# Performance work log

Measured on AMD Instinct MI355X. Metric: run time of the kernel, lower is better.

Reference implementation:

```python
import jax, jax.numpy as jnp
import numpy as np

B, N, EB, NA, DIM, NIT = 256, 128, 5, 64, 512, 3  # EB = n_bonds + 1 (channel 0 = no-bond, dropped)


def setup_inputs() -> dict:
    key = jax.random.key(0)
    ks = jax.random.split(key, 10)
    adj = jax.random.uniform(ks[0], (B, N, N, EB), dtype=jnp.float32)
    node = jax.random.normal(ks[1], (B, N, NA), dtype=jnp.float32)
    hidden = jnp.zeros((B, N, DIM), dtype=jnp.float32)  # accepted but unused by forward
    # nn.Linear default init: U(-1/sqrt(fan_in), 1/sqrt(fan_in))
    se = 1.0 / np.sqrt(NA)
    sd = 1.0 / np.sqrt(DIM)
    W_embed = jax.random.uniform(ks[2], (NA, DIM), minval=-se, maxval=se, dtype=jnp.float32)
    b_embed = jax.random.uniform(ks[3], (DIM,), minval=-se, maxval=se, dtype=jnp.float32)
    W_layers = jax.random.uniform(ks[4], (NIT, DIM, DIM), minval=-sd, maxval=sd, dtype=jnp.float32)
    b_layers = jax.random.uniform(ks[5], (NIT, DIM), minval=-sd, maxval=sd, dtype=jnp.float32)
    W_out = jax.random.uniform(ks[6], (DIM, 1), minval=-sd, maxval=sd, dtype=jnp.float32)
    b_out = jax.random.uniform(ks[7], (1,), minval=-sd, maxval=sd, dtype=jnp.float32)
    return {"adj": adj, "hidden": hidden, "node": node,
            "W_embed": W_embed, "b_embed": b_embed,
            "W_layers": W_layers, "b_layers": b_layers,
            "W_out": W_out, "b_out": b_out}


def reference(adj, hidden, node, W_embed, b_embed, W_layers, b_layers, W_out, b_out):
    # adj[:, :, :, 1:].permute(0, 3, 1, 2) -> [B, E, N, N]
    a = jnp.transpose(adj[..., 1:], (0, 3, 1, 2))
    h = node @ W_embed + b_embed  # [B, N, DIM]
    for i in range(NIT):  # WLSLinearLayer: relu(Linear(h + sum_e adj_e @ h))
        agg = jnp.einsum('benm,bmd->bnd', a, h)  # sum over bond types of neighbor aggregation
        h = jax.nn.relu((h + agg) @ W_layers[i] + b_layers[i])
    graph_repr = jnp.mean(h, axis=1)  # [B, DIM]
    logit = graph_repr @ W_out + b_out  # [B, 1], activation=None path
    return (logit, graph_repr)
```

## Files before the change

### kernel.cpp

```cpp
#include <hip/hip_runtime.h>
#include <hip/hip_bf16.h>


typedef __bf16 bf16;
typedef __bf16 bf16x4 __attribute__((ext_vector_type(4)));
typedef __bf16 bf16x8 __attribute__((ext_vector_type(8)));
typedef float floatx4 __attribute__((ext_vector_type(4)));


__global__ __launch_bounds__(256) void k_pack(const float* __restrict__ We,
                                              const float* __restrict__ Wl,
                                              bf16* __restrict__ PWe,
                                              bf16* __restrict__ PWl) {
    __shared__ float S[512][17];
    int z = blockIdx.y, td = blockIdx.x;
    const float* src; bf16* dst; int K;
    if (z < 3) { src = Wl + (size_t)z * 262144; dst = PWl + (size_t)z * 262144; K = 512; }
    else       { src = We;                      dst = PWe;                      K = 64; }
    int tid = threadIdx.x;
    int x = tid & 15, y = tid >> 4;
    for (int kb = 0; kb < K; kb += 16) {
        int k = kb + y;
        S[k][x] = src[(size_t)k * 512 + td * 16 + x];
    }
    __syncthreads();
    int lane = tid & 63, w = tid >> 6, q = lane >> 4, l16 = lane & 15;
    int KT = K >> 5;
    for (int tk = w; tk < KT; tk += 4) {
        bf16x8 v;
#pragma unroll
        for (int j = 0; j < 8; j++) v[j] = (bf16)S[tk * 32 + q * 8 + j][l16];
        *(bf16x8*)&dst[(size_t)((td * KT + tk) * 64 + lane) * 8] = v;
    }
}

__global__ __launch_bounds__(1024, 4) void k_mega(
    const float* __restrict__ adj,
    const float* __restrict__ nodef,
    const bf16* __restrict__ PWe,
    const float* __restrict__ b_embed,
    const bf16* __restrict__ PWl,
    const float* __restrict__ b_layers,
    const float* __restrict__ W_out,
    const float* __restrict__ b_out,
    float* __restrict__ out)
{
    __shared__ __align__(16) char pool[163840];
    bf16* HT = (bf16*)pool;
    bf16* AhatP = (bf16*)(pool + 131072);

    const int b = blockIdx.x;
    const int tid = threadIdx.x;
    const int lane = tid & 63, wid = tid >> 6;
    const int q = lane >> 4, l16 = lane & 15;

    {
        const float4* srcb = (const float4*)(adj + (size_t)b * 81920);
#pragma unroll
        for (int p = 0; p < 4; p++) {
            int t = p * 1024 + tid;
            const float4* ptr = srcb + (size_t)t * 5;
            float4 v0 = ptr[0], v1 = ptr[1], v2 = ptr[2], v3 = ptr[3], v4 = ptr[4];
            float s0 = v0.y + v0.z + v0.w + v1.x;
            float s1 = v1.z + v1.w + v2.x + v2.y;
            float s2 = v2.w + v3.x + v3.y + v3.z;
            float s3 = v4.x + v4.y + v4.z + v4.w;
            int n = t >> 5, m0 = (t & 31) * 4;
            bf16x4 o;
            o[0] = (bf16)(s0 + ((n == m0 + 0) ? 1.f : 0.f));
            o[1] = (bf16)(s1 + ((n == m0 + 1) ? 1.f : 0.f));
            o[2] = (bf16)(s2 + ((n == m0 + 2) ? 1.f : 0.f));
            o[3] = (bf16)(s3 + ((n == m0 + 3) ? 1.f : 0.f));
            int ntG = n >> 4, l16n = n & 15;
            int kk = m0 >> 5, mq = (m0 & 31) >> 3, half = (m0 >> 2) & 1;
            int cphys = mq * 16 + (l16n ^ (mq * 2));
            *(bf16x4*)&AhatP[(size_t)(((ntG * 4 + kk) * 64 + cphys) * 8 + half * 4)] = o;
        }
    }

    {
        const float* Ab = nodef + (size_t)b * 8192;
        floatx4 accE[8][2] = {};
#pragma unroll
        for (int kk = 0; kk < 2; kk++) {
            bf16x8 bfr[2];
#pragma unroll
            for (int nt = 0; nt < 2; nt++)
                bfr[nt] = *(const bf16x8*)&PWe[(size_t)(((wid * 2 + nt) * 2 + kk) * 64 + lane) * 8];
#pragma unroll
            for (int half = 0; half < 2; half++) {
                bf16x8 af[4];
#pragma unroll
                for (int mt = 0; mt < 4; mt++) {
                    const float* srcp = Ab + (size_t)((half * 4 + mt) * 16 + l16) * 64 + kk * 32 + q * 8;
                    float4 x = *(const float4*)srcp;
                    float4 y = *(const float4*)(srcp + 4);
                    bf16x8 v;
                    v[0] = (bf16)x.x; v[1] = (bf16)x.y; v[2] = (bf16)x.z; v[3] = (bf16)x.w;
                    v[4] = (bf16)y.x; v[5] = (bf16)y.y; v[6] = (bf16)y.z; v[7] = (bf16)y.w;
                    af[mt] = v;
                }
#pragma unroll
                for (int mt = 0; mt < 4; mt++)
#pragma unroll
                    for (int nt = 0; nt < 2; nt++)
                        accE[half * 4 + mt][nt] = __builtin_amdgcn_mfma_f32_16x16x32_bf16(af[mt], bfr[nt], accE[half * 4 + mt][nt], 0, 0, 0);
            }
        }
#pragma unroll
        for (int nt = 0; nt < 2; nt++) {
            int d = wid * 32 + nt * 16 + l16;
            float bv = b_embed[d];
#pragma unroll
            for (int mt = 0; mt < 8; mt++) {
                int c = mt * 2 + (q >> 1);
                int off = ((c ^ (d & 15)) << 3) + (q & 1) * 4;
                bf16x4 pk;
#pragma unroll
                for (int r = 0; r < 4; r++) pk[r] = (bf16)(accE[mt][nt][r] + bv);
                *(bf16x4*)&HT[d * 128 + off] = pk;
            }
        }
    }
    __syncthreads();

    const int pc = lane ^ ((lane >> 4) * 2);

    for (int it = 0; it < 3; it++) {
        const bf16* WT = PWl + (size_t)it * 262144;
        const float* bl = b_layers + it * 512;

        const bf16* Wb0 = WT + (size_t)(wid * 2 + 0) * 8192 + lane * 8;
        const bf16* Wb1 = WT + (size_t)(wid * 2 + 1) * 8192 + lane * 8;

        bf16x8 w00 = *(const bf16x8*)Wb0;
        bf16x8 w01 = *(const bf16x8*)Wb1;
        bf16x8 w10 = *(const bf16x8*)(Wb0 + 512);
        bf16x8 w11 = *(const bf16x8*)(Wb1 + 512);

        floatx4 at[2][8] = {};
#pragma unroll
        for (int kk = 0; kk < 4; kk++) {
            bf16x8 afr[2];
#pragma unroll
            for (int dt = 0; dt < 2; dt++) {
                int drow = wid * 32 + dt * 16 + l16;
                int off = ((4 * kk + q) ^ (drow & 15)) << 3;
                afr[dt] = *(const bf16x8*)&HT[drow * 128 + off];
            }
#pragma unroll
            for (int g = 0; g < 2; g++) {
                bf16x8 bfr[4];
#pragma unroll
                for (int nt = 0; nt < 4; nt++)
                    bfr[nt] = *(const bf16x8*)&AhatP[(size_t)(((g * 4 + nt) * 4 + kk) * 64 + pc) * 8];
                __builtin_amdgcn_s_setprio(1);
#pragma unroll
                for (int nt = 0; nt < 4; nt++)
#pragma unroll
                    for (int dt = 0; dt < 2; dt++)
                        at[dt][g * 4 + nt] = __builtin_amdgcn_mfma_f32_16x16x32_bf16(afr[dt], bfr[nt], at[dt][g * 4 + nt], 0, 0, 0);
                __builtin_amdgcn_s_setprio(0);
            }
        }
        {
            bf16* Treg = HT + wid * 4096;
#pragma unroll
            for (int dt = 0; dt < 2; dt++)
#pragma unroll
                for (int nt = 0; nt < 8; nt++) {
                    int n = nt * 16 + l16;
                    bf16x4 pk;
#pragma unroll
                    for (int r = 0; r < 4; r++) pk[r] = (bf16)at[dt][nt][r];
                    *(bf16x4*)&Treg[(dt * 2 + (q >> 1)) * 1024 + n * 8 + (q & 1) * 4] = pk;
                }
        }
        __syncthreads();

        floatx4 acc[8][2] = {};
        for (int dc = 0; dc < 16; dc++) {
            int dcn = (dc + 2) & 15;
            bf16x8 n0 = *(const bf16x8*)(Wb0 + dcn * 512);
            bf16x8 n1 = *(const bf16x8*)(Wb1 + dcn * 512);
            const bf16* Tdc = HT + dc * 4096 + q * 1024 + l16 * 8;
            bf16x8 afa[4];
#pragma unroll
            for (int mt = 0; mt < 4; mt++)
                afa[mt] = *(const bf16x8*)&Tdc[mt * 128];
            __builtin_amdgcn_s_setprio(1);
#pragma unroll
            for (int mt = 0; mt < 4; mt++)
                acc[mt][0] = __builtin_amdgcn_mfma_f32_16x16x32_bf16(afa[mt], w00, acc[mt][0], 0, 0, 0);
#pragma unroll
            for (int mt = 0; mt < 4; mt++)
                acc[mt][1] = __builtin_amdgcn_mfma_f32_16x16x32_bf16(afa[mt], w01, acc[mt][1], 0, 0, 0);
            __builtin_amdgcn_s_setprio(0);
            bf16x8 afb[4];
#pragma unroll
            for (int mt = 0; mt < 4; mt++)
                afb[mt] = *(const bf16x8*)&Tdc[(mt + 4) * 128];
            __builtin_amdgcn_s_setprio(1);
#pragma unroll
            for (int mt = 0; mt < 4; mt++)
                acc[mt + 4][0] = __builtin_amdgcn_mfma_f32_16x16x32_bf16(afb[mt], w00, acc[mt + 4][0], 0, 0, 0);
#pragma unroll
            for (int mt = 0; mt < 4; mt++)
                acc[mt + 4][1] = __builtin_amdgcn_mfma_f32_16x16x32_bf16(afb[mt], w01, acc[mt + 4][1], 0, 0, 0);
            __builtin_amdgcn_s_setprio(0);
            w00 = w10; w01 = w11; w10 = n0; w11 = n1;
        }

        if (it < 2) {
            __syncthreads();
#pragma unroll
            for (int nt = 0; nt < 2; nt++) {
                int dp = wid * 32 + nt * 16 + l16;
                float bv = bl[dp];
#pragma unroll
                for (int mt = 0; mt < 8; mt++) {
                    int c = mt * 2 + (q >> 1);
                    int off = ((c ^ (dp & 15)) << 3) + (q & 1) * 4;
                    bf16x4 pk;
#pragma unroll
                    for (int r = 0; r < 4; r++) pk[r] = (bf16)fmaxf(acc[mt][nt][r] + bv, 0.f);
                    *(bf16x4*)&HT[dp * 128 + off] = pk;
                }
            }
        } else {
            float* RsF = (float*)(pool + 131072);
#pragma unroll
            for (int nt = 0; nt < 2; nt++) {
                int dp = wid * 32 + nt * 16 + l16;
                float bv = bl[dp];
                float s = 0.f;
#pragma unroll
                for (int mt = 0; mt < 8; mt++)
#pragma unroll
                    for (int r = 0; r < 4; r++)
                        s += fmaxf(acc[mt][nt][r] + bv, 0.f);
                s += __shfl_down(s, 32);
                s += __shfl_down(s, 16);
                if (lane < 16) RsF[dp] = s;
            }
        }
    }
    __syncthreads();

    float* RsF = (float*)(pool + 131072);
    float* lpF = (float*)(pool + 131072 + 2048);
    if (tid < 512) {
        float g = RsF[tid] * (1.f / 128.f);
        out[256 + (size_t)b * 512 + tid] = g;
        lpF[tid] = g * W_out[tid];
    }
    __syncthreads();
    if (wid == 0) {
        float s = 0.f;
#pragma unroll
        for (int k = 0; k < 8; k++) s += lpF[lane + k * 64];
        s += __shfl_down(s, 32);
        s += __shfl_down(s, 16);
        s += __shfl_down(s, 8);
        s += __shfl_down(s, 4);
        s += __shfl_down(s, 2);
        s += __shfl_down(s, 1);
        if (lane == 0) out[b] = s + b_out[0];
    }
}

extern "C" void kernel_launch(void* const* d_in, const int* in_sizes, int n_in,
                              void* d_out, int out_size, void* d_ws, size_t ws_size,
                              hipStream_t stream) {
    const float* adj      = (const float*)d_in[0];
    const float* node     = (const float*)d_in[2];
    const float* W_embed  = (const float*)d_in[3];
    const float* b_embed  = (const float*)d_in[4];
    const float* W_layers = (const float*)d_in[5];
    const float* b_layers = (const float*)d_in[6];
    const float* W_out    = (const float*)d_in[7];
    const float* b_out    = (const float*)d_in[8];
    float* out = (float*)d_out;

    char* ws = (char*)d_ws;
    bf16* PWe = (bf16*)(ws);
    bf16* PWl = (bf16*)(ws + 65536);

    k_pack<<<dim3(32, 4), 256, 0, stream>>>(W_embed, W_layers, PWe, PWl);
    k_mega<<<256, 1024, 0, stream>>>(adj, node, PWe, b_embed, PWl, b_layers,
                                     W_out, b_out, out);
}
```

Baseline: 231.6 us.

## Stagger weight-chunk order per wave and start own chunk before barrier

Each wave now walks the 16 d-chunks of the second GEMM in rotated order starting at its own chunk. It processes that chunk, which it wrote itself, before the __syncthreads, so some MFMA work overlaps the barrier wait, and the rotation spreads LDS bank access across waves. The final mean/W_out products are also computed directly in the last-iteration epilogue, which removes one barrier and the extra LDS pass. The cost is more index arithmetic and a duplicated loop body, which may raise register pressure.

```diff
diff --git a/kernel.cpp b/kernel.cpp
--- a/kernel.cpp
+++ b/kernel.cpp
@@ -133,10 +133,10 @@
         const bf16* Wb0 = WT + (size_t)(wid * 2 + 0) * 8192 + lane * 8;
         const bf16* Wb1 = WT + (size_t)(wid * 2 + 1) * 8192 + lane * 8;
 
-        bf16x8 w00 = *(const bf16x8*)Wb0;
-        bf16x8 w01 = *(const bf16x8*)Wb1;
-        bf16x8 w10 = *(const bf16x8*)(Wb0 + 512);
-        bf16x8 w11 = *(const bf16x8*)(Wb1 + 512);
+        bf16x8 w00 = *(const bf16x8*)(Wb0 + wid * 512);
+        bf16x8 w01 = *(const bf16x8*)(Wb1 + wid * 512);
+        bf16x8 w10 = *(const bf16x8*)(Wb0 + ((wid + 1) & 15) * 512);
+        bf16x8 w11 = *(const bf16x8*)(Wb1 + ((wid + 1) & 15) * 512);
 
         floatx4 at[2][8] = {};
 #pragma unroll
@@ -176,11 +176,45 @@
                     *(bf16x4*)&Treg[(dt * 2 + (q >> 1)) * 1024 + n * 8 + (q & 1) * 4] = pk;
                 }
         }
+
+        floatx4 acc[8][2] = {};
+
+        {
+            int dcn = (wid + 2) & 15;
+            bf16x8 n0 = *(const bf16x8*)(Wb0 + dcn * 512);
+            bf16x8 n1 = *(const bf16x8*)(Wb1 + dcn * 512);
+            const bf16* Tdc = HT + wid * 4096 + q * 1024 + l16 * 8;
+            bf16x8 afa[4];
+#pragma unroll
+            for (int mt = 0; mt < 4; mt++)
+                afa[mt] = *(const bf16x8*)&Tdc[mt * 128];
+            __builtin_amdgcn_s_setprio(1);
+#pragma unroll
+            for (int mt = 0; mt < 4; mt++)
+                acc[mt][0] = __builtin_amdgcn_mfma_f32_16x16x32_bf16(afa[mt], w00, acc[mt][0], 0, 0, 0);
+#pragma unroll
+            for (int mt = 0; mt < 4; mt++)
+                acc[mt][1] = __builtin_amdgcn_mfma_f32_16x16x32_bf16(afa[mt], w01, acc[mt][1], 0, 0, 0);
+            __builtin_amdgcn_s_setprio(0);
+            bf16x8 afb[4];
+#pragma unroll
+            for (int mt = 0; mt < 4; mt++)
+                afb[mt] = *(const bf16x8*)&Tdc[(mt + 4) * 128];
+            __builtin_amdgcn_s_setprio(1);
+#pragma unroll
+            for (int mt = 0; mt < 4; mt++)
+                acc[mt + 4][0] = __builtin_amdgcn_mfma_f32_16x16x32_bf16(afb[mt], w00, acc[mt + 4][0], 0, 0, 0);
+#pragma unroll
+            for (int mt = 0; mt < 4; mt++)
+                acc[mt + 4][1] = __builtin_amdgcn_mfma_f32_16x16x32_bf16(afb[mt], w01, acc[mt + 4][1], 0, 0, 0);
+            __builtin_amdgcn_s_setprio(0);
+            w00 = w10; w01 = w11; w10 = n0; w11 = n1;
+        }
         __syncthreads();
 
-        floatx4 acc[8][2] = {};
-        for (int dc = 0; dc < 16; dc++) {
-            int dcn = (dc + 2) & 15;
+        for (int i = 1; i < 16; i++) {
+            int dc = (wid + i) & 15;
+            int dcn = (wid + i + 2) & 15;
             bf16x8 n0 = *(const bf16x8*)(Wb0 + dcn * 512);
             bf16x8 n1 = *(const bf16x8*)(Wb1 + dcn * 512);
             const bf16* Tdc = HT + dc * 4096 + q * 1024 + l16 * 8;
@@ -228,7 +262,7 @@
                 }
             }
         } else {
-            float* RsF = (float*)(pool + 131072);
+            float* lpF = (float*)(pool + 131072);
 #pragma unroll
             for (int nt = 0; nt < 2; nt++) {
                 int dp = wid * 32 + nt * 16 + l16;
@@ -241,21 +275,18 @@
                         s += fmaxf(acc[mt][nt][r] + bv, 0.f);
                 s += __shfl_down(s, 32);
                 s += __shfl_down(s, 16);
-                if (lane < 16) RsF[dp] = s;
+                if (lane < 16) {
+                    float g = s * (1.f / 128.f);
+                    out[256 + (size_t)b * 512 + dp] = g;
+                    lpF[dp] = g * W_out[dp];
+                }
             }
         }
     }
     __syncthreads();
 
-    float* RsF = (float*)(pool + 131072);
-    float* lpF = (float*)(pool + 131072 + 2048);
-    if (tid < 512) {
-        float g = RsF[tid] * (1.f / 128.f);
-        out[256 + (size_t)b * 512 + tid] = g;
-        lpF[tid] = g * W_out[tid];
-    }
-    __syncthreads();
     if (wid == 0) {
+        float* lpF = (float*)(pool + 131072);
         float s = 0.f;
 #pragma unroll
         for (int k = 0; k < 8; k++) s += lpF[lane + k * 64];
```

Measured after the change: 244.2 us. 5.5% more time.
